# Kernel optimization log

Hardware: AMD Instinct MI355X
Metric: run time of the kernel (lower is better)

## Reference

```python
import math
import jax, jax.numpy as jnp
import numpy as np

N_DIM = 1024
N_HEADS = 16
HEAD_DIM = N_DIM // N_HEADS
B, S = 8, 1024


def setup_inputs() -> dict:
    key = jax.random.key(0)
    ks = jax.random.split(key, 10)
    s = 1.0 / math.sqrt(N_DIM)
    inp = {
        "x": jax.random.normal(ks[0], (B, S, N_DIM), dtype=jnp.float32),
        "padding_mask": jax.random.randint(ks[1], (B, 1, 1, S), 0, 2).astype(bool),
        "Wq": jax.random.uniform(ks[2], (N_DIM, N_DIM), jnp.float32, -s, s),
        "bq": jax.random.uniform(ks[3], (N_DIM,), jnp.float32, -s, s),
        "Wk": jax.random.uniform(ks[4], (N_DIM, N_DIM), jnp.float32, -s, s),
        "bk": jax.random.uniform(ks[5], (N_DIM,), jnp.float32, -s, s),
        "Wv": jax.random.uniform(ks[6], (N_DIM, N_DIM), jnp.float32, -s, s),
        "bv": jax.random.uniform(ks[7], (N_DIM,), jnp.float32, -s, s),
        "Wo": jax.random.uniform(ks[8], (N_DIM, N_DIM), jnp.float32, -s, s),
        "bo": jax.random.uniform(ks[9], (N_DIM,), jnp.float32, -s, s),
    }
    return inp


def _split_heads(t):
    b, s, _ = t.shape
    return t.reshape(b, s, N_HEADS, HEAD_DIM).transpose(0, 2, 1, 3)  # [B,H,S,D]


def reference(x, padding_mask, Wq, bq, Wk, bk, Wv, bv, Wo, bo):
    # nn.Linear: y = x @ W^T + b
    Q = _split_heads(x @ Wq.T + bq)
    K = _split_heads(x @ Wk.T + bk)
    V = _split_heads(x @ Wv.T + bv)
    scale = 1.0 / math.sqrt(HEAD_DIM)
    scores = jnp.einsum('bhqd,bhkd->bhqk', Q, K) * scale
    scores = jnp.where(padding_mask, -jnp.inf, scores)
    attn = jax.nn.softmax(scores, axis=-1)
    attn = jnp.nan_to_num(attn, nan=0.0)  # fully-masked rows -> 0
    ctx = jnp.einsum('bhqk,bhkd->bhqd', attn, V)
    ctx = ctx.transpose(0, 2, 1, 3).reshape(x.shape[0], x.shape[1], N_DIM)
    return ctx @ Wo.T + bo  # dropout is identity in eval mode
```

## Files before the change

### kernel.cpp

```cpp
#include <hip/hip_runtime.h>
#include <hip/hip_bf16.h>
#include <math.h>

#define B_SZ 8
#define SEQ 1024
#define NDIM 1024
#define NH 16
#define HD 64
#define MROWS (B_SZ * SEQ)
#define SCALE_L2E 0.18033688011112042f
#define NEGB (-1e30f)

typedef __attribute__((ext_vector_type(4))) float f32x4;
typedef __attribute__((ext_vector_type(8))) short s16x8;
typedef __attribute__((ext_vector_type(4))) short s16x4;

#define MFMA16(a, b, c) __builtin_amdgcn_mfma_f32_16x16x32_bf16((a), (b), (c), 0, 0, 0)

__device__ __forceinline__ unsigned short f2bf(float f) {
    union { float f; unsigned int u; } v; v.f = f;
    unsigned int r = v.u + 0x7FFFu + ((v.u >> 16) & 1u);
    return (unsigned short)(r >> 16);
}
__device__ __forceinline__ unsigned short f2bf_t(float f) {
    union { float f; unsigned int u; } v; v.f = f;
    return (unsigned short)(v.u >> 16);
}

__device__ __forceinline__ void llds16(const void* g, void* l) {
    __builtin_amdgcn_global_load_lds(
        (const __attribute__((address_space(1))) void*)g,
        (__attribute__((address_space(3))) void*)l, 16, 0, 0);
}

__global__ void prep_mask(const unsigned char* __restrict__ m, float* __restrict__ bias) {
    __shared__ int fl[3];
    if (threadIdx.x < 3) fl[threadIdx.x] = 0;
    __syncthreads();
    int a = 0, o1 = 0, o23 = 0;
    for (int i = threadIdx.x; i < B_SZ * SEQ; i += 1024) {
        unsigned char v = m[i];
        if (v) { int q = i & 3; if (q == 0) a = 1; else if (q == 1) o1 = 1; else o23 = 1; }
    }
    if (a)   atomicOr(&fl[0], 1);
    if (o1)  atomicOr(&fl[1], 1);
    if (o23) atomicOr(&fl[2], 1);
    __syncthreads();
    int fmt;
    if (fl[0] && !fl[1] && !fl[2])      fmt = 0;
    else if (!fl[0] && !fl[1] && fl[2]) fmt = 2;
    else                                fmt = 1;
    for (int i = threadIdx.x; i < B_SZ * SEQ; i += 1024) {
        int t;
        if (fmt == 0)      t = ((const int*)m)[i];
        else if (fmt == 1) t = m[i];
        else               t = (((const float*)m)[i] != 0.f);
        bias[i] = t ? NEGB : 0.f;
    }
}

__global__ void cvt_all(const float* __restrict__ x,
                        const float* __restrict__ wq, const float* __restrict__ wk,
                        const float* __restrict__ wv, const float* __restrict__ wo,
                        unsigned short* __restrict__ xbf, unsigned short* __restrict__ wbf)
{
    const int bid = blockIdx.x;
    if (bid < MROWS * NDIM / 1024) {
        const int i = bid * 1024 + threadIdx.x * 4;
        float4 v = *(const float4*)(x + i);
        s16x4 o; o[0] = (short)f2bf(v.x); o[1] = (short)f2bf(v.y);
        o[2] = (short)f2bf(v.z); o[3] = (short)f2bf(v.w);
        *(s16x4*)(xbf + i) = o;
    } else {
        const int j = (bid - MROWS * NDIM / 1024) * 1024 + threadIdx.x * 4;
        const int which = j >> 20;
        const float* s = (which == 0) ? wq : (which == 1) ? wk : (which == 2) ? wv : wo;
        float4 v = *(const float4*)(s + (j & ((1 << 20) - 1)));
        s16x4 o; o[0] = (short)f2bf(v.x); o[1] = (short)f2bf(v.y);
        o[2] = (short)f2bf(v.z); o[3] = (short)f2bf(v.w);
        *(s16x4*)(wbf + j) = o;
    }
}

#define GBM 128
#define GBK 64

#define STAGE_TILE(lds, src)                                              \
    {                                                                     \
_Pragma("unroll")                                                         \
        for (int i = 0; i < 4; ++i) {                                     \
            const int s = tid + i * 256;                                  \
            const int r = s >> 3, c = s & 7;                              \
            llds16((src) + (size_t)r * NDIM + ((c ^ (r & 7)) * 8),        \
                   &(lds)[s * 8]);                                        \
        }                                                                 \
    }

__device__ __forceinline__ void gemm_core(
    const unsigned short* __restrict__ Xp, const unsigned short* __restrict__ Wp,
    short* As, short* Bs, int tid, int wm, int wn, int g, int ql,
    f32x4 acc[4][4])
{
    for (int k0 = 0; k0 < NDIM; k0 += GBK) {
        STAGE_TILE(As, Xp + k0)
        STAGE_TILE(Bs, Wp + k0)
        __syncthreads();
#pragma unroll
        for (int kk = 0; kk < 2; ++kk) {
            s16x8 af[4], bf[4];
#pragma unroll
            for (int f = 0; f < 4; ++f) {
                const int ra = wm * 64 + f * 16 + ql;
                const int rb = wn * 64 + f * 16 + ql;
                af[f] = *(const s16x8*)&As[ra * 64 + (((kk * 4 + g) ^ (ra & 7)) * 8)];
                bf[f] = *(const s16x8*)&Bs[rb * 64 + (((kk * 4 + g) ^ (rb & 7)) * 8)];
            }
#pragma unroll
            for (int i = 0; i < 4; ++i)
#pragma unroll
                for (int j = 0; j < 4; ++j)
                    acc[i][j] = MFMA16(af[i], bf[j], acc[i][j]);
        }
        __syncthreads();
    }
}

__global__ __launch_bounds__(256) void gemm_qkv(
    const unsigned short* __restrict__ X, const unsigned short* __restrict__ Wb,
    const float* __restrict__ bq, const float* __restrict__ bk, const float* __restrict__ bv,
    unsigned short* __restrict__ Qo, unsigned short* __restrict__ Ko,
    unsigned short* __restrict__ Vt)
{
    __shared__ __align__(16) short As[GBM * GBK];
    __shared__ __align__(16) short Bs[GBM * GBK];

    const int tid = threadIdx.x, lane = tid & 63, w = tid >> 6;
    const int wm = w >> 1, wn = w & 1;
    const int g = lane >> 4, ql = lane & 15;
    const int which = blockIdx.y >> 3, ny = blockIdx.y & 7;
    const int bm = blockIdx.x * GBM, bn = ny * GBM;
    const unsigned short* W = Wb + (size_t)which * (1 << 20);
    const float* bias = (which == 0) ? bq : (which == 1) ? bk : bv;

    f32x4 acc[4][4] = {};
    gemm_core(X + (size_t)bm * NDIM, W + (size_t)bn * NDIM,
              As, Bs, tid, wm, wn, g, ql, acc);

    if (which < 2) {
        unsigned short* O = (which == 0) ? Qo : Ko;
#pragma unroll
        for (int j = 0; j < 4; ++j) {
            const int col = bn + wn * 64 + j * 16 + ql;
            const float bv_ = bias[col];
#pragma unroll
            for (int i = 0; i < 4; ++i) {
                const int row0 = bm + wm * 64 + i * 16 + 4 * g;
#pragma unroll
                for (int r = 0; r < 4; ++r)
                    O[(size_t)(row0 + r) * NDIM + col] = f2bf(acc[i][j][r] + bv_);
            }
        }
    } else {
#pragma unroll
        for (int j = 0; j < 4; ++j) {
            const int col = bn + wn * 64 + j * 16 + ql;
            const float bv_ = bias[col];
            const int h = col >> 6, dd = col & 63;
#pragma unroll
            for (int i = 0; i < 4; ++i) {
                const int row0 = bm + wm * 64 + i * 16 + 4 * g;
                const int b_ = row0 >> 10, s_ = row0 & 1023;
                s16x4 pk;
#pragma unroll
                for (int r = 0; r < 4; ++r) pk[r] = (short)f2bf(acc[i][j][r] + bv_);
                *(s16x4*)&Vt[(((size_t)(b_ * NH + h)) * HD + dd) * SEQ + s_] = pk;
            }
        }
    }
}

__global__ __launch_bounds__(256) void gemm_out(
    const unsigned short* __restrict__ X, const unsigned short* __restrict__ W,
    const float* __restrict__ bias, float* __restrict__ out)
{
    __shared__ __align__(16) short As[GBM * GBK];
    __shared__ __align__(16) short Bs[GBM * GBK];

    const int tid = threadIdx.x, lane = tid & 63, w = tid >> 6;
    const int wm = w >> 1, wn = w & 1;
    const int g = lane >> 4, ql = lane & 15;
    const int bm = blockIdx.x * GBM, bn = blockIdx.y * GBM;

    f32x4 acc[4][4] = {};
    gemm_core(X + (size_t)bm * NDIM, W + (size_t)bn * NDIM,
              As, Bs, tid, wm, wn, g, ql, acc);

#pragma unroll
    for (int j = 0; j < 4; ++j) {
        const int col = bn + wn * 64 + j * 16 + ql;
        const float bv_ = bias[col];
#pragma unroll
        for (int i = 0; i < 4; ++i) {
            const int row0 = bm + wm * 64 + i * 16 + 4 * g;
#pragma unroll
            for (int r = 0; r < 4; ++r)
                out[(size_t)(row0 + r) * NDIM + col] = acc[i][j][r] + bv_;
        }
    }
}

#define KVB 128

__global__ __launch_bounds__(256) void attn(
    const unsigned short* __restrict__ Q, const unsigned short* __restrict__ K,
    const unsigned short* __restrict__ Vt, const float* __restrict__ maskB,
    unsigned short* __restrict__ ctx)
{
    __shared__ __align__(16) short Ks[KVB * 64];
    __shared__ __align__(16) short Vs[80 * KVB];
    __shared__ __align__(16) short Ps[4][16 * 72];

    const int tid = threadIdx.x, lane = tid & 63, w = tid >> 6;
    const int g = lane >> 4, ql = lane & 15;
    const int bh = blockIdx.x, b = bh >> 4, h = bh & 15;
    const int q0 = blockIdx.y * 64;

    {
        const int r = 64 + (tid >> 4), c = (tid & 15) * 8;
        const short v = (r == 64) ? (short)0x3F80 : (short)0;
        s16x8 pk = {v, v, v, v, v, v, v, v};
        *(s16x8*)&Vs[r * KVB + c] = pk;
    }

    const size_t qrow = (size_t)(b * SEQ + q0 + w * 16 + ql) * NDIM + h * HD;
    const s16x8 qa0 = *(const s16x8*)&Q[qrow + g * 8];
    const s16x8 qa1 = *(const s16x8*)&Q[qrow + 32 + g * 8];

    f32x4 o[5] = {};

    const unsigned short* Kb = K + (size_t)(b * SEQ) * NDIM + h * HD;
    const unsigned short* Vb = Vt + (size_t)bh * HD * SEQ;
    const float* mb = maskB + b * SEQ;
    short* Pp = &Ps[w][0];

    for (int kt = 0; kt < SEQ / KVB; ++kt) {
        const int kv0 = kt * KVB;
        s16x8 kr[4], vr[4];
#pragma unroll
        for (int i = 0; i < 4; ++i) {
            const int s = tid + i * 256;
            const int rk = s >> 3, ck = s & 7;
            const int rv = s >> 4, cv = s & 15;
            kr[i] = *(const s16x8*)&Kb[(size_t)(kv0 + rk) * NDIM + ck * 8];
            vr[i] = *(const s16x8*)&Vb[(size_t)rv * SEQ + kv0 + cv * 8];
        }
        __syncthreads();
#pragma unroll
        for (int i = 0; i < 4; ++i) {
            const int s = tid + i * 256;
            const int rk = s >> 3, ck = s & 7;
            const int rv = s >> 4, cv = s & 15;
            *(s16x8*)&Ks[rk * 64 + ((ck ^ (rk & 7)) * 8)] = kr[i];
            *(s16x8*)&Vs[rv * KVB + ((cv ^ (rv & 7)) * 8)] = vr[i];
        }
        __syncthreads();

        f32x4 sa[8] = {};
#pragma unroll
        for (int nt = 0; nt < 8; ++nt) {
            const int row = nt * 16 + ql;
            const s16x8 kb0 = *(const s16x8*)&Ks[row * 64 + (((g)     ^ (row & 7)) * 8)];
            const s16x8 kb1 = *(const s16x8*)&Ks[row * 64 + (((4 + g) ^ (row & 7)) * 8)];
            sa[nt] = MFMA16(qa0, kb0, sa[nt]);
            sa[nt] = MFMA16(qa1, kb1, sa[nt]);
        }

#pragma unroll
        for (int h2 = 0; h2 < 2; ++h2) {
#pragma unroll
            for (int n4 = 0; n4 < 4; ++n4) {
                const int nt = h2 * 4 + n4;
                const float mbv = mb[kv0 + nt * 16 + ql];
#pragma unroll
                for (int r = 0; r < 4; ++r) {
                    const float p = exp2f(fmaf(sa[nt][r], SCALE_L2E, mbv));
                    Pp[(4 * g + r) * 72 + n4 * 16 + ql] = (short)f2bf_t(p);
                }
            }
            const s16x8 pa0 = *(const s16x8*)&Pp[ql * 72 + 8 * g];
            const s16x8 pa1 = *(const s16x8*)&Pp[ql * 72 + 32 + 8 * g];
#pragma unroll
            for (int dt = 0; dt < 5; ++dt) {
                const int row = dt * 16 + ql;
                const s16x8 vb0 = *(const s16x8*)&Vs[row * KVB + (((h2 * 8 + g)     ^ (row & 7)) * 8)];
                const s16x8 vb1 = *(const s16x8*)&Vs[row * KVB + (((h2 * 8 + 4 + g) ^ (row & 7)) * 8)];
                o[dt] = MFMA16(pa0, vb0, o[dt]);
                o[dt] = MFMA16(pa1, vb1, o[dt]);
            }
        }
    }

    const int lsrc = lane & 48;
#pragma unroll
    for (int r = 0; r < 4; ++r) {
        const float lval = __shfl(o[4][r], lsrc);
        const float inv = (lval > 0.f) ? 1.f / lval : 0.f;
        const size_t row = (size_t)(b * SEQ + q0 + w * 16 + 4 * g + r) * NDIM + h * HD;
#pragma unroll
        for (int dt = 0; dt < 4; ++dt)
            ctx[row + dt * 16 + ql] = f2bf(o[dt][r] * inv);
    }
}

extern "C" void kernel_launch(void* const* d_in, const int* in_sizes, int n_in,
                              void* d_out, int out_size, void* d_ws, size_t ws_size,
                              hipStream_t stream)
{
    (void)in_sizes; (void)n_in; (void)out_size; (void)ws_size;
    const float* x  = (const float*)d_in[0];
    const unsigned char* mask = (const unsigned char*)d_in[1];
    const float* Wq = (const float*)d_in[2];
    const float* bq = (const float*)d_in[3];
    const float* Wk = (const float*)d_in[4];
    const float* bk = (const float*)d_in[5];
    const float* Wv = (const float*)d_in[6];
    const float* bv = (const float*)d_in[7];
    const float* Wo = (const float*)d_in[8];
    const float* bo = (const float*)d_in[9];
    float* out = (float*)d_out;

    char* ws = (char*)d_ws;
    float*          maskB = (float*)ws;
    unsigned short* xbf   = (unsigned short*)(ws + (32 << 10));
    unsigned short* wbf   = xbf + (size_t)MROWS * NDIM;
    unsigned short* Qbf   = wbf + (size_t)4 * NDIM * NDIM;
    unsigned short* Kbf   = Qbf + (size_t)MROWS * NDIM;
    unsigned short* Vtb   = Kbf + (size_t)MROWS * NDIM;
    unsigned short* Cbf   = Vtb + (size_t)MROWS * NDIM;

    prep_mask<<<1, 1024, 0, stream>>>(mask, maskB);
    cvt_all<<<(MROWS * NDIM + 4 * NDIM * NDIM) / 1024, 256, 0, stream>>>(
        x, Wq, Wk, Wv, Wo, xbf, wbf);

    gemm_qkv<<<dim3(MROWS / GBM, 24), 256, 0, stream>>>(xbf, wbf, bq, bk, bv,
                                                        Qbf, Kbf, Vtb);
    attn<<<dim3(B_SZ * NH, SEQ / 64), 256, 0, stream>>>(Qbf, Kbf, Vtb, maskB, Cbf);
    gemm_out<<<dim3(MROWS / GBM, NDIM / GBM), 256, 0, stream>>>(
        Cbf, wbf + (size_t)3 * NDIM * NDIM, bo, out);
}
```

Baseline: 287.8 us.

## Software-pipeline K/V prefetch in attention with smaller KV tiles and MFMA priority

Halves the attention KV tile from 128 to 64 keys and double-buffers the K/V global loads in registers, so the next tile's loads are issued before the current tile's compute. It also raises wave priority around the MFMA blocks with s_setprio. The intent is to hide global-load latency behind compute. In exchange there are twice as many tiles and barriers, and more registers are live at once.

```diff
diff --git a/kernel.cpp b/kernel.cpp
--- a/kernel.cpp
+++ b/kernel.cpp
@@ -209,7 +209,8 @@
     }
 }
 
-#define KVB 128
+#define KVB 64
+#define NKT (SEQ / KVB)
 
 __global__ __launch_bounds__(256) void attn(
     const unsigned short* __restrict__ Q, const unsigned short* __restrict__ K,
@@ -217,7 +218,7 @@
     unsigned short* __restrict__ ctx)
 {
     __shared__ __align__(16) short Ks[KVB * 64];
-    __shared__ __align__(16) short Vs[80 * KVB];
+    __shared__ __align__(16) short Vs[80 * 64];
     __shared__ __align__(16) short Ps[4][16 * 72];
 
     const int tid = threadIdx.x, lane = tid & 63, w = tid >> 6;
@@ -226,10 +227,10 @@
     const int q0 = blockIdx.y * 64;
 
     {
-        const int r = 64 + (tid >> 4), c = (tid & 15) * 8;
+        const int r = 64 + (tid >> 4), c = (tid & 15) * 4;
         const short v = (r == 64) ? (short)0x3F80 : (short)0;
-        s16x8 pk = {v, v, v, v, v, v, v, v};
-        *(s16x8*)&Vs[r * KVB + c] = pk;
+        s16x4 pk = {v, v, v, v};
+        *(s16x4*)&Vs[r * 64 + c] = pk;
     }
 
     const size_t qrow = (size_t)(b * SEQ + q0 + w * 16 + ql) * NDIM + h * HD;
@@ -243,62 +244,74 @@
     const float* mb = maskB + b * SEQ;
     short* Pp = &Ps[w][0];
 
-    for (int kt = 0; kt < SEQ / KVB; ++kt) {
-        const int kv0 = kt * KVB;
-        s16x8 kr[4], vr[4];
-#pragma unroll
-        for (int i = 0; i < 4; ++i) {
-            const int s = tid + i * 256;
-            const int rk = s >> 3, ck = s & 7;
-            const int rv = s >> 4, cv = s & 15;
-            kr[i] = *(const s16x8*)&Kb[(size_t)(kv0 + rk) * NDIM + ck * 8];
-            vr[i] = *(const s16x8*)&Vb[(size_t)rv * SEQ + kv0 + cv * 8];
-        }
-        __syncthreads();
-#pragma unroll
-        for (int i = 0; i < 4; ++i) {
-            const int s = tid + i * 256;
-            const int rk = s >> 3, ck = s & 7;
-            const int rv = s >> 4, cv = s & 15;
-            *(s16x8*)&Ks[rk * 64 + ((ck ^ (rk & 7)) * 8)] = kr[i];
-            *(s16x8*)&Vs[rv * KVB + ((cv ^ (rv & 7)) * 8)] = vr[i];
-        }
-        __syncthreads();
-
-        f32x4 sa[8] = {};
-#pragma unroll
-        for (int nt = 0; nt < 8; ++nt) {
-            const int row = nt * 16 + ql;
-            const s16x8 kb0 = *(const s16x8*)&Ks[row * 64 + (((g)     ^ (row & 7)) * 8)];
-            const s16x8 kb1 = *(const s16x8*)&Ks[row * 64 + (((4 + g) ^ (row & 7)) * 8)];
-            sa[nt] = MFMA16(qa0, kb0, sa[nt]);
-            sa[nt] = MFMA16(qa1, kb1, sa[nt]);
-        }
-
-#pragma unroll
-        for (int h2 = 0; h2 < 2; ++h2) {
-#pragma unroll
-            for (int n4 = 0; n4 < 4; ++n4) {
-                const int nt = h2 * 4 + n4;
-                const float mbv = mb[kv0 + nt * 16 + ql];
-#pragma unroll
-                for (int r = 0; r < 4; ++r) {
-                    const float p = exp2f(fmaf(sa[nt][r], SCALE_L2E, mbv));
-                    Pp[(4 * g + r) * 72 + n4 * 16 + ql] = (short)f2bf_t(p);
-                }
-            }
-            const s16x8 pa0 = *(const s16x8*)&Pp[ql * 72 + 8 * g];
-            const s16x8 pa1 = *(const s16x8*)&Pp[ql * 72 + 32 + 8 * g];
-#pragma unroll
-            for (int dt = 0; dt < 5; ++dt) {
-                const int row = dt * 16 + ql;
-                const s16x8 vb0 = *(const s16x8*)&Vs[row * KVB + (((h2 * 8 + g)     ^ (row & 7)) * 8)];
-                const s16x8 vb1 = *(const s16x8*)&Vs[row * KVB + (((h2 * 8 + 4 + g) ^ (row & 7)) * 8)];
-                o[dt] = MFMA16(pa0, vb0, o[dt]);
-                o[dt] = MFMA16(pa1, vb1, o[dt]);
-            }
-        }
-    }
+    s16x8 ka[2], va[2], kb2[2], vb2[2];
+
+#pragma unroll
+    for (int i = 0; i < 2; ++i) {
+        const int s = tid + i * 256, rk = s >> 3, ck = s & 7;
+        ka[i] = *(const s16x8*)&Kb[(size_t)rk * NDIM + ck * 8];
+        va[i] = *(const s16x8*)&Vb[(size_t)rk * SEQ + ck * 8];
+    }
+
+#define ATTN_TILE(KIN, VIN, KOUT, VOUT, KT, DO_LOAD)                          \
+    {                                                                         \
+        __syncthreads();                    \
+        _Pragma("unroll")                                                     \
+        for (int i = 0; i < 2; ++i) {                                         \
+            const int s = tid + i * 256, rk = s >> 3, ck = s & 7;             \
+            *(s16x8*)&Ks[rk * 64 + ((ck ^ (rk & 7)) * 8)] = KIN[i];           \
+            *(s16x8*)&Vs[rk * 64 + ((ck ^ (rk & 7)) * 8)] = VIN[i];           \
+        }                                                                     \
+        if (DO_LOAD) {                 \
+            const int kvn = ((KT) + 1) * KVB;                                 \
+            _Pragma("unroll")                                                 \
+            for (int i = 0; i < 2; ++i) {                                     \
+                const int s = tid + i * 256, rk = s >> 3, ck = s & 7;         \
+                KOUT[i] = *(const s16x8*)&Kb[(size_t)(kvn + rk) * NDIM + ck * 8]; \
+                VOUT[i] = *(const s16x8*)&Vb[(size_t)rk * SEQ + kvn + ck * 8];    \
+            }                                                                 \
+        }                                                                     \
+        __syncthreads();                       \
+        const int kv0 = (KT) * KVB;                                           \
+        f32x4 sa[4] = {};                                                     \
+        __builtin_amdgcn_s_setprio(1);                                        \
+        _Pragma("unroll")                                                     \
+        for (int nt = 0; nt < 4; ++nt) {                                      \
+            const int row = nt * 16 + ql;                                     \
+            const s16x8 kf0 = *(const s16x8*)&Ks[row * 64 + (((g)     ^ (row & 7)) * 8)]; \
+            const s16x8 kf1 = *(const s16x8*)&Ks[row * 64 + (((4 + g) ^ (row & 7)) * 8)]; \
+            sa[nt] = MFMA16(qa0, kf0, sa[nt]);                                \
+            sa[nt] = MFMA16(qa1, kf1, sa[nt]);                                \
+        }                                                                     \
+        __builtin_amdgcn_s_setprio(0);                                        \
+        _Pragma("unroll")                                                     \
+        for (int nt = 0; nt < 4; ++nt) {                                      \
+            const float mbv = mb[kv0 + nt * 16 + ql];                         \
+            _Pragma("unroll")                                                 \
+            for (int r = 0; r < 4; ++r) {                                     \
+                const float p = exp2f(fmaf(sa[nt][r], SCALE_L2E, mbv));       \
+                Pp[(4 * g + r) * 72 + nt * 16 + ql] = (short)f2bf_t(p);       \
+            }                                                                 \
+        }                                                                     \
+        const s16x8 pa0 = *(const s16x8*)&Pp[ql * 72 + 8 * g];                \
+        const s16x8 pa1 = *(const s16x8*)&Pp[ql * 72 + 32 + 8 * g];           \
+        __builtin_amdgcn_s_setprio(1);                                        \
+        _Pragma("unroll")                                                     \
+        for (int dt = 0; dt < 5; ++dt) {                                      \
+            const int row = dt * 16 + ql;                                     \
+            const s16x8 vf0 = *(const s16x8*)&Vs[row * 64 + (((g)     ^ (row & 7)) * 8)]; \
+            const s16x8 vf1 = *(const s16x8*)&Vs[row * 64 + (((4 + g) ^ (row & 7)) * 8)]; \
+            o[dt] = MFMA16(pa0, vf0, o[dt]);                                  \
+            o[dt] = MFMA16(pa1, vf1, o[dt]);                                  \
+        }                                                                     \
+        __builtin_amdgcn_s_setprio(0);                                        \
+    }
+
+    for (int kt2 = 0; kt2 < NKT / 2; ++kt2) {
+        ATTN_TILE(ka,  va,  kb2, vb2, 2 * kt2,     1)
+        ATTN_TILE(kb2, vb2, ka,  va,  2 * kt2 + 1, (kt2 < NKT / 2 - 1))
+    }
+#undef ATTN_TILE
 
     const int lsrc = lane & 48;
 #pragma unroll
```

Result: faster. 272.2 us (-5.4%).
